# Kernel optimization log

Measured on AMD Instinct MI355X. Metric: run time of the kernel, lower is better.

The kernel has to match this reference:

```python
import jax, jax.numpy as jnp
import numpy as np

# All BatchNorms are in inference mode: folded to per-channel affine (g, b)
# where g = gamma/sqrt(running_var+eps), b = beta - running_mean*g.

def _conv(x, w, stride=1, pad=0, groups=1):
    return jax.lax.conv_general_dilated(
        x, w, (stride, stride), ((pad, pad), (pad, pad)),
        dimension_numbers=('NCHW', 'OIHW', 'NCHW'), feature_group_count=groups)

def _bn(x, g, b):
    return x * g[None, :, None, None] + b[None, :, None, None]

def _gn(x, g, b, eps=1e-5):
    # GroupNorm with 1 group: normalize over (C,H,W) per sample
    m = jnp.mean(x, axis=(1, 2, 3), keepdims=True)
    v = jnp.var(x, axis=(1, 2, 3), keepdims=True)
    return (x - m) * jax.lax.rsqrt(v + eps) * g[None, :, None, None] + b[None, :, None, None]

def _maxpool3(x):
    return jax.lax.reduce_window(x, -jnp.inf, jax.lax.max,
                                 (1, 1, 3, 3), (1, 1, 1, 1),
                                 ((0, 0), (0, 0), (1, 1), (1, 1)))


def reference(x, w_stem, g_stem, b_stem,
              w_cb1, g_cb1, b_cb1, w_cb2, g_cb2, b_cb2, w_cb3, g_cb3, b_cb3,
              w_cbres, g_cbres, b_cbres,
              w_lvc, g_lvc, b_lvc, codewords, cw_scale, g_enc, b_enc,
              w_fc, b_fc,
              gn1_g, gn1_b, w_dw, g_dw, b_dw, w_pw, g_pw, b_pw,
              gn2_g, gn2_b, w_fc1, bias_fc1, w_fc2, bias_fc2, ls1, ls2,
              w_cnv1, b_cnv1):
    relu = jax.nn.relu
    C = x.shape[1]
    # ---- stem: 7x7 conv + BN + ReLU + 3x3 maxpool (stride 1) ----
    x1 = _maxpool3(relu(_bn(_conv(x, w_stem, pad=3), g_stem, b_stem)))

    # ================= LVC branch =================
    # ConvBlock (res_conv=True, stride=1)
    t = relu(_bn(_conv(x1, w_cb1), g_cb1, b_cb1))           # 1x1 C->C/4
    t = relu(_bn(_conv(t, w_cb2, pad=1), g_cb2, b_cb2))     # 3x3 C/4->C/4
    t = _bn(_conv(t, w_cb3), g_cb3, b_cb3)                  # 1x1 C/4->C
    res = _bn(_conv(x1, w_cbres), g_cbres, b_cbres)         # 1x1 residual
    xc = relu(t + res)

    # LVC: 1x1 conv + BN + ReLU -> Encoding -> BN1d -> ReLU -> mean over codes
    z = relu(_bn(_conv(xc, w_lvc), g_lvc, b_lvc))
    b_, _, H, W = z.shape
    zf = z.reshape(b_, C, H * W).transpose(0, 2, 1)         # (b, N, C)
    # scaled L2: scale_k * ||x_n - c_k||^2, expanded (no (b,N,K,C) tensor)
    x2 = jnp.sum(zf * zf, axis=-1, keepdims=True)           # (b, N, 1)
    c2 = jnp.sum(codewords * codewords, axis=-1)            # (K,)
    dist = cw_scale * (x2 - 2.0 * jnp.einsum('bnc,kc->bnk', zf, codewords) + c2)
    A = jax.nn.softmax(dist, axis=2)                        # (b, N, K)
    # aggregate: sum_n A * (x - c) = A^T x - (sum_n A) * c
    en = jnp.einsum('bnk,bnc->bkc', A, zf) - A.sum(axis=1)[..., None] * codewords
    en = relu(en * g_enc[None, :, None] + b_enc[None, :, None])  # BN1d over codes
    en = en.mean(axis=1)                                    # (b, C)
    gam = jax.nn.sigmoid(en @ w_fc.T + b_fc)                # (b, C)
    x_lvc = relu(xc + xc * gam[:, :, None, None])

    # ================= LightMLP branch =================
    h = _gn(x1, gn1_g, gn1_b)
    h = jax.nn.silu(_bn(_conv(h, w_dw, groups=C), g_dw, b_dw))   # depthwise 1x1
    h = jax.nn.silu(_bn(_conv(h, w_pw), g_pw, b_pw))             # pointwise 1x1
    xm = x1 + ls1[None, :, None, None] * h
    h2 = _gn(xm, gn2_g, gn2_b)
    h2 = jax.nn.gelu(_conv(h2, w_fc1) + bias_fc1[None, :, None, None], approximate=False)
    h2 = _conv(h2, w_fc2) + bias_fc2[None, :, None, None]
    xm = xm + ls2[None, :, None, None] * h2

    # ---- fuse: concat + 1x1 conv ----
    out = _conv(jnp.concatenate([x_lvc, xm], axis=1), w_cnv1) + b_cnv1[None, :, None, None]
    return out


def setup_inputs() -> dict:
    B, C, H, W, K = 8, 256, 40, 40, 64
    c = C // 4
    HID = 4 * C
    key = jax.random.key(0)
    ks = iter(jax.random.split(key, 80))
    rn = lambda *s: jax.random.normal(next(ks), s, jnp.float32)
    un = lambda lo, hi, *s: jax.random.uniform(next(ks), s, jnp.float32, lo, hi)

    def aff(n):
        return un(0.8, 1.2, n), rn(n) * 0.1

    d = {}
    d['x'] = rn(B, C, H, W)
    d['w_stem'] = rn(C, C, 7, 7) * 0.01
    d['g_stem'], d['b_stem'] = aff(C)
    d['w_cb1'] = rn(c, C, 1, 1) * 0.05
    d['g_cb1'], d['b_cb1'] = aff(c)
    d['w_cb2'] = rn(c, c, 3, 3) * 0.05
    d['g_cb2'], d['b_cb2'] = aff(c)
    d['w_cb3'] = rn(C, c, 1, 1) * 0.05
    d['g_cb3'], d['b_cb3'] = aff(C)
    d['w_cbres'] = rn(C, C, 1, 1) * 0.05
    d['g_cbres'], d['b_cbres'] = aff(C)
    d['w_lvc'] = rn(C, C, 1, 1) * 0.05
    d['g_lvc'], d['b_lvc'] = aff(C)
    std = 1.0 / (K * C) ** 0.5
    d['codewords'] = un(-std, std, K, C)
    d['cw_scale'] = un(-1.0, 0.0, K)
    d['g_enc'], d['b_enc'] = aff(K)
    d['w_fc'] = rn(C, C) * 0.05
    d['b_fc'] = rn(C) * 0.1
    d['gn1_g'], d['gn1_b'] = aff(C)
    d['w_dw'] = rn(C, 1, 1, 1) * 0.5
    d['g_dw'], d['b_dw'] = aff(C)
    d['w_pw'] = rn(C, C, 1, 1) * 0.05
    d['g_pw'], d['b_pw'] = aff(C)
    d['gn2_g'], d['gn2_b'] = aff(C)
    d['w_fc1'] = rn(HID, C, 1, 1) * 0.05
    d['bias_fc1'] = rn(HID) * 0.02
    d['w_fc2'] = rn(C, HID, 1, 1) * 0.02
    d['bias_fc2'] = rn(C) * 0.02
    d['ls1'] = rn(C) * 0.1
    d['ls2'] = rn(C) * 0.1
    d['w_cnv1'] = rn(C, 2 * C, 1, 1) * 0.04
    d['b_cnv1'] = rn(C) * 0.02
    return d
```

## Files before the change

### kernel.cpp

```cpp
#include <hip/hip_runtime.h>
#include <hip/hip_bf16.h>
#include <math.h>

typedef unsigned short u16;
typedef u16 u16x4 __attribute__((ext_vector_type(4)));
typedef u16 u16x8 __attribute__((ext_vector_type(8)));
typedef short s16x8 __attribute__((ext_vector_type(8)));
typedef float f32x4 __attribute__((ext_vector_type(4)));

#define DEVI static __device__ __forceinline__

DEVI float bf2f(u16 u){ unsigned v=((unsigned)u)<<16; float f; __builtin_memcpy(&f,&v,4); return f; }
DEVI u16 f2bf(float f){ unsigned u; __builtin_memcpy(&u,&f,4); u=(u+0x7FFFu+((u>>16)&1u))>>16; return (u16)u; }

DEVI void gload16(const u16* g, u16* l){
  __builtin_amdgcn_global_load_lds(
      (const __attribute__((address_space(1))) void*)(unsigned long long)g,
      (__attribute__((address_space(3))) void*)(unsigned int)(unsigned long long)l,
      16, 0, 0);
}

constexpr size_t AL(size_t x){ return (x+511)&~(size_t)511; }
constexpr size_t sACT =8ull*1600*256*2;
constexpr size_t oXPAD=0;                constexpr size_t sXPAD=8ull*46*46*256*2;
constexpr size_t oT1P =AL(oXPAD+sXPAD);  constexpr size_t sT1P=8ull*42*42*64*2;
constexpr size_t oSTAT=AL(oT1P+sT1P);    constexpr size_t sSTAT=512;
constexpr size_t ZERO_BYTES=oSTAT+sSTAT;
constexpr size_t oWST =AL(ZERO_BYTES);   constexpr size_t sWST=6553600;
constexpr size_t oWCB2=AL(oWST+sWST);    constexpr size_t sWCB2=9*64*64*2;
constexpr size_t oWSM =AL(oWCB2+sWCB2);  constexpr size_t sWSM=901120ull*2;
constexpr size_t oC2  =AL(oWSM+sWSM);    constexpr size_t sC2=1024;
constexpr size_t oSTEM=AL(oC2+sC2);
constexpr size_t oX1  =AL(oSTEM+sACT);
constexpr size_t oT2  =AL(oX1+sACT);     constexpr size_t sT2=8ull*1600*64*2;
constexpr size_t oRRES=AL(oT2+sT2);
constexpr size_t oXC  =AL(oRRES+sACT);
constexpr size_t oZ   =AL(oXC+sACT);
constexpr size_t oZT  =AL(oZ+sACT);
constexpr size_t oX2  =AL(oZT+sACT);     constexpr size_t sX2=12800*4;
constexpr size_t oDOT =AL(oX2+sX2);      constexpr size_t sDOT=12800ull*64*4;
constexpr size_t oAS  =AL(oDOT+sDOT);    constexpr size_t sAS=64ull*12800*2;
constexpr size_t oASUM=AL(oAS+sAS);      constexpr size_t sASUM=512*4;
constexpr size_t oEN  =AL(oASUM+sASUM);  constexpr size_t sEN=8ull*64*256*4;
constexpr size_t oENM =AL(oEN+sEN);      constexpr size_t sENM=8*256*4;
constexpr size_t oGAM =AL(oENM+sENM);    constexpr size_t sGAM=8*256*4;
constexpr size_t oH2A =AL(oGAM+sGAM);    constexpr size_t sH2A=8ull*1600*1024*2;
constexpr size_t oFUSE=AL(oH2A+sH2A);    constexpr size_t sFUSE=8ull*1600*512*2;
constexpr size_t TOTAL_WS=oFUSE+sFUSE;
static_assert(TOTAL_WS < ((size_t)120<<20), "ws layout ~94MB");
constexpr size_t oPART =oRRES;             constexpr size_t sPART =4ull*12800*256*4;
constexpr size_t oPART2=oPART+sPART;       constexpr size_t sPART2=3ull*12800*64*4;
static_assert(oPART2+sPART2<=TOTAL_WS, "partials fit");

struct WCP { const float* s[9]; u16* d[9]; };
__global__ void wcast_plain(WCP p){
  int idx=blockIdx.x*256+threadIdx.x;
  int j,rel;
  if(idx<16384){j=0;rel=idx;}
  else if(idx<32768){j=1;rel=idx-16384;}
  else if(idx<98304){j=2;rel=idx-32768;}
  else if(idx<163840){j=3;rel=idx-98304;}
  else if(idx<229376){j=4;rel=idx-163840;}
  else if(idx<491520){j=5;rel=idx-229376;}
  else if(idx<753664){j=6;rel=idx-491520;}
  else if(idx<884736){j=7;rel=idx-753664;}
  else if(idx<901120){j=8;rel=idx-884736;}
  else return;
  p.d[j][rel]=f2bf(p.s[j][rel]);
}
__global__ void wcast_stem(const float* __restrict__ w, u16* __restrict__ o){
  __shared__ u16 sh[49*256];
  int co=blockIdx.x, ci=threadIdx.x;
  const float* src=w+(size_t)(co*256+ci)*49;
#pragma unroll 7
  for(int j=0;j<49;j++) sh[j*256+ci]=f2bf(src[j]);
  __syncthreads();
#pragma unroll 7
  for(int j=0;j<49;j++) o[((size_t)j*256+co)*256+ci]=sh[j*256+ci];
}
__global__ void wcast_cb2(const float* __restrict__ w, u16* __restrict__ o){
  int idx=blockIdx.x*256+threadIdx.x;
  if(idx>=9*4096) return;
  int ci=idx&63; int t=idx>>6; int co=t&63; int dhw=t>>6;
  o[idx]=f2bf(w[(co*64+ci)*9+dhw]);
}
__global__ void c2k(const float* __restrict__ cw, float* __restrict__ c2){
  int k=threadIdx.x; if(k>=64) return;
  float s=0.f;
  for(int i=0;i<256;i++){ float v=cw[k*256+i]; s+=v*v; }
  c2[k]=s;
}

__global__ void x_to_xpad(const float* __restrict__ x, u16* __restrict__ xpad){
  __shared__ u16 sh[40*257];
  int h=blockIdx.x, z=blockIdx.y;
  const float* xb=x+(size_t)z*409600+h*40;
  for(int e=threadIdx.x;e<10240;e+=256){ int c=e/40, w=e-40*(e/40); sh[w*257+c]=f2bf(xb[c*1600+w]); }
  __syncthreads();
  u16* op=xpad+((size_t)(z*46+h+3)*46+3)*256;
  for(int e=threadIdx.x;e<10240;e+=256){ int w=e>>8, c=e&255; op[w*256+c]=sh[w*257+c]; }
}

template<int COT,int COTOT,int PXT,int CIN,int PW,int KS,int NW,int TPS,int TTOT>
__global__ __launch_bounds__(NW*64) void conv_lds(
    const u16* __restrict__ Xp, const u16* __restrict__ Wt, float* __restrict__ part){
  constexpr int WPN=PXT/64;
  constexpr int IW=(COT/16)/NW;
  constexpr int IA=(PXT/16)/NW;
  constexpr int CST=CIN/32;
  constexpr int CSH=(CST==8)?3:1;

  __shared__ __align__(16) u16 sW[2][COT*32];
  __shared__ __align__(16) u16 sA[2][PXT*32];

  const int wv=threadIdx.x>>6, ln=threadIdx.x&63, lr=ln&15, kg=ln>>4;
  const int wr=wv/WPN, wc=wv%WPN;
  const int co0=blockIdx.x*COT;
  const int px0=blockIdx.y*PXT;
  const int slice=blockIdx.z;
  const int tb=slice*TPS;
  const int te=(slice==gridDim.z-1)?TTOT:(tb+TPS);
  const int nst=(te-tb)<<CSH;

  int wbase[IW], abase[IA];
#pragma unroll
  for(int q=0;q<IW;q++){
    int wrow=(wv*IW+q)*16+(ln>>2);
    wbase[q]=(co0+wrow)*CIN+(ln&3)*8;
  }
#pragma unroll
  for(int q=0;q<IA;q++){
    int p=px0+(wv*IA+q)*16+(ln>>2);
    int z=p/1600, rem=p-z*1600;
    int h=rem/40, w=rem-h*40;
    abase[q]=((z*PW+h)*PW+w)*CIN+(ln&3)*8;
  }

  f32x4 acc[4][4];
#pragma unroll
  for(int i=0;i<4;i++)
#pragma unroll
    for(int j=0;j<4;j++) acc[i][j]=f32x4{0.f,0.f,0.f,0.f};

  auto stage=[&](int buf,int s){
    int ti=tb+(s>>CSH);
    int c0=(s&(CST-1))<<5;
    int dh=ti/KS, dw=ti-dh*KS;
    const u16* wsrc=Wt+(size_t)ti*COTOT*CIN+c0;
    int aoff=(dh*PW+dw)*CIN+c0;
#pragma unroll
    for(int q=0;q<IW;q++) gload16(wsrc+wbase[q], &sW[buf][(wv*IW+q)*512]);
#pragma unroll
    for(int q=0;q<IA;q++) gload16(Xp+abase[q]+aoff, &sA[buf][(wv*IA+q)*512]);
  };
  auto compute=[&](int buf){
    s16x8 av[4], bv[4];
    const u16* wb=&sW[buf][(wr*64+lr)*32+kg*8];
    const u16* ab=&sA[buf][(wc*64+lr)*32+kg*8];
#pragma unroll
    for(int i=0;i<4;i++) av[i]=*(const s16x8*)(wb+i*512);
#pragma unroll
    for(int j=0;j<4;j++) bv[j]=*(const s16x8*)(ab+j*512);
#pragma unroll
    for(int i=0;i<4;i++)
#pragma unroll
      for(int j=0;j<4;j++)
        acc[i][j]=__builtin_amdgcn_mfma_f32_16x16x32_bf16(av[i],bv[j],acc[i][j],0,0,0);
  };

  stage(0,0);
  for(int s=0;s<nst;s++){
    __syncthreads();
    if(s+1<nst) stage((s+1)&1, s+1);
    compute(s&1);
  }

  float* pb=part+(size_t)slice*12800*COTOT;
#pragma unroll
  for(int i=0;i<4;i++){
    int co=co0+wr*64+i*16+kg*4;
#pragma unroll
    for(int j=0;j<4;j++){
      int px=px0+wc*64+j*16+lr;
      *(f32x4*)(pb+(size_t)px*COTOT+co)=acc[i][j];
    }
  }
}

template<int MT8,int NS>
__global__ void ep_red(const float* __restrict__ part, const float* __restrict__ g,
    const float* __restrict__ b, u16* __restrict__ out){
  int t=blockIdx.x*256+threadIdx.x;
  int c=(t%MT8)*8; int gp=t/MT8;
  size_t base=(size_t)gp*(MT8*8)+c;
  constexpr size_t SS=(size_t)12800*MT8*8;
  f32x4 v0=*(const f32x4*)(part+base), v1=*(const f32x4*)(part+base+4);
#pragma unroll
  for(int s=1;s<NS;s++){
    f32x4 a0=*(const f32x4*)(part+s*SS+base), a1=*(const f32x4*)(part+s*SS+base+4);
#pragma unroll
    for(int q=0;q<4;q++){ v0[q]+=a0[q]; v1[q]+=a1[q]; }
  }
  u16x8 o;
#pragma unroll
  for(int q=0;q<4;q++) o[q]  =f2bf(fmaxf(v0[q]*g[c+q]  +b[c+q],  0.f));
#pragma unroll
  for(int q=0;q<4;q++) o[4+q]=f2bf(fmaxf(v1[q]*g[c+4+q]+b[c+4+q],0.f));
  *(u16x8*)(out+base)=o;
}

__global__ void maxpool3(const u16* __restrict__ in, u16* __restrict__ out){
  int t=blockIdx.x*256+threadIdx.x;
  int c8=(t&31)*8; int gp=t>>5;
  int n=gp%1600; int z=gp/1600; int h=n/40, w=n%40;
  float mx[8];
#pragma unroll
  for(int q=0;q<8;q++) mx[q]=-1e30f;
  for(int dh=-1;dh<=1;dh++){ int hh=h+dh; if((unsigned)hh>=40u) continue;
    for(int dw=-1;dw<=1;dw++){ int ww=w+dw; if((unsigned)ww>=40u) continue;
      u16x8 v=*(const u16x8*)(in+((size_t)z*1600+hh*40+ww)*256+c8);
#pragma unroll
      for(int q=0;q<8;q++) mx[q]=fmaxf(mx[q],bf2f(v[q]));
    }}
  u16x8 o;
#pragma unroll
  for(int q=0;q<8;q++) o[q]=f2bf(mx[q]);
  *(u16x8*)(out+((size_t)z*1600+n)*256+c8)=o;
}

struct GP {
  const u16* A; long long Asz; int lda;
  const u16* Bp; long long Bsz; int ldb;
  int Kd;
  const float *e0,*e1,*e2,*e3;
  const u16* r0;
  u16* ob; float* of; u16* ob2;
  int ldo;
};

template<int MF,int NF,int EPI>
__global__ __launch_bounds__(256) void gemm_nt(GP p){
  const int wv=threadIdx.x>>6, ln=threadIdx.x&63, lr=ln&15, kg=ln>>4;
  int z=blockIdx.z, kc=0;
  if constexpr(EPI==11){ kc=z%5; z=z/5; }
  const int m0=blockIdx.x*(MF*64)+wv*(MF*16);
  const int n0=blockIdx.y*(NF*16);
  const u16* A=p.A+(size_t)z*p.Asz+kc*320;
  const u16* Bb=p.Bp+(size_t)z*p.Bsz+kc*320;
  const u16* ar[MF]; const u16* br[NF];
#pragma unroll
  for(int i=0;i<MF;i++) ar[i]=A+(size_t)(m0+i*16+lr)*p.lda+kg*8;
#pragma unroll
  for(int j=0;j<NF;j++) br[j]=Bb+(size_t)(n0+j*16+lr)*p.ldb+kg*8;
  f32x4 acc[MF][NF];
#pragma unroll
  for(int i=0;i<MF;i++)
#pragma unroll
    for(int j=0;j<NF;j++) acc[i][j]=f32x4{0.f,0.f,0.f,0.f};
  for(int k=0;k<p.Kd;k+=32){
    s16x8 av[MF], bv[NF];
#pragma unroll
    for(int i=0;i<MF;i++) av[i]=*(const s16x8*)(ar[i]+k);
#pragma unroll
    for(int j=0;j<NF;j++) bv[j]=*(const s16x8*)(br[j]+k);
#pragma unroll
    for(int i=0;i<MF;i++)
#pragma unroll
      for(int j=0;j<NF;j++)
        acc[i][j]=__builtin_amdgcn_mfma_f32_16x16x32_bf16(av[i],bv[j],acc[i][j],0,0,0);
  }
#pragma unroll
  for(int i=0;i<MF;i++){
    const int mb=m0+i*16+kg*4;
#pragma unroll
    for(int j=0;j<NF;j++){
      const int n=n0+j*16+lr;
      f32x4 v=acc[i][j];
      if constexpr(EPI==1){
        int h=n/40, w=n%40;
        u16x4 o;
#pragma unroll
        for(int q=0;q<4;q++) o[q]=f2bf(fmaxf(v[q]*p.e0[mb+q]+p.e1[mb+q],0.f));
        *(u16x4*)(p.ob+((size_t)z*1764+(h+1)*42+(w+1))*64+mb)=o;
      } else if constexpr(EPI==2){
        u16x4 o;
#pragma unroll
        for(int q=0;q<4;q++) o[q]=f2bf(v[q]*p.e0[mb+q]+p.e1[mb+q]);
        *(u16x4*)(p.ob+((size_t)z*1600+n)*256+mb)=o;
      } else if constexpr(EPI==3){
        u16x4 rv=*(const u16x4*)(p.r0+((size_t)z*1600+n)*256+mb);
        u16x4 o;
#pragma unroll
        for(int q=0;q<4;q++) o[q]=f2bf(fmaxf(v[q]*p.e0[mb+q]+p.e1[mb+q]+bf2f(rv[q]),0.f));
        *(u16x4*)(p.ob+((size_t)z*1600+n)*256+mb)=o;
      } else if constexpr(EPI==4){
        u16x4 o;
#pragma unroll
        for(int q=0;q<4;q++) o[q]=f2bf(fmaxf(v[q]*p.e0[mb+q]+p.e1[mb+q],0.f));
        *(u16x4*)(p.ob+((size_t)z*1600+n)*256+mb)=o;
#pragma unroll
        for(int q=0;q<4;q++) p.ob2[((size_t)z*256+mb+q)*1600+n]=o[q];
      } else if constexpr(EPI==5){
#pragma unroll
        for(int q=0;q<4;q++) p.of[(size_t)(mb+q)*64+n]=v[q];
      } else if constexpr(EPI==7){
        u16x4 o;
#pragma unroll
        for(int q=0;q<4;q++){ float t=v[q]+p.e0[mb+q]; t=0.5f*t*(1.f+erff(t*0.70710678f)); o[q]=f2bf(t); }
        *(u16x4*)(p.ob+((size_t)z*1600+n)*p.ldo+mb)=o;
      } else if constexpr(EPI==8){
        u16x4 rv=*(const u16x4*)(p.r0+((size_t)z*1600+n)*256+mb);
        u16x4 o;
#pragma unroll
        for(int q=0;q<4;q++){ float t=v[q]+p.e0[mb+q]; o[q]=f2bf(bf2f(rv[q])+p.e1[mb+q]*t); }
        *(u16x4*)(p.ob+((size_t)z*1600+n)*512+mb)=o;
      } else if constexpr(EPI==9){
        u16x4 rv=*(const u16x4*)(p.r0+((size_t)z*1600+n)*256+mb);
        u16x4 o;
#pragma unroll
        for(int q=0;q<4;q++){ float t=v[q]*p.e0[mb+q]+p.e1[mb+q]; float s=t/(1.f+expf(-t));
          o[q]=f2bf(bf2f(rv[q])+p.e2[mb+q]*s); }
        *(u16x4*)(p.ob+((size_t)z*1600+n)*256+mb)=o;
      } else if constexpr(EPI==10){
#pragma unroll
        for(int q=0;q<4;q++) p.of[((size_t)z*256+mb+q)*1600+n]=v[q]+p.e0[mb+q];
      } else if constexpr(EPI==11){
#pragma unroll
        for(int q=0;q<4;q++) atomicAdd(&p.of[((size_t)z*64+mb+q)*256+n],v[q]);
      }
    }
  }
}

__global__ void rowsq(const u16* __restrict__ zb, float* __restrict__ x2){
  int wv=threadIdx.x>>6, ln=threadIdx.x&63;
  int gp=blockIdx.x*4+wv;
  u16x4 v=*(const u16x4*)(zb+(size_t)gp*256+ln*4);
  float s=0.f;
#pragma unroll
  for(int q=0;q<4;q++){ float f=bf2f(v[q]); s+=f*f; }
  for(int d=32;d;d>>=1) s+=__shfl_xor(s,d);
  if(ln==0) x2[gp]=s;
}

__global__ void softmax_k(const float* __restrict__ dot, const float* __restrict__ x2,
    const float* __restrict__ c2, const float* __restrict__ cws, u16* __restrict__ As){
  int wv=threadIdx.x>>6, ln=threadIdx.x&63;
  int base=blockIdx.x*64+wv*16;
  float sc=cws[ln], cc=c2[ln];
  for(int it=0;it<16;it++){
    int gp=base+it;
    float d=sc*(x2[gp]-2.f*dot[(size_t)gp*64+ln]+cc);
    float m=d;
    for(int o=32;o;o>>=1) m=fmaxf(m,__shfl_xor(m,o));
    float e=expf(d-m);
    float s=e;
    for(int o=32;o;o>>=1) s+=__shfl_xor(s,o);
    As[(size_t)ln*12800+gp]=f2bf(e/s);
  }
}

__global__ void asum_k(const u16* __restrict__ As, float* __restrict__ Asum){
  int wv=threadIdx.x>>6, ln=threadIdx.x&63;
  int id=blockIdx.x*4+wv;
  int b=id>>6, k=id&63;
  const u16* r=As+(size_t)k*12800+b*1600;
  float s=0.f;
  for(int i=ln;i<1600;i+=64) s+=bf2f(r[i]);
  for(int o=32;o;o>>=1) s+=__shfl_xor(s,o);
  if(ln==0) Asum[id]=s;
}

__global__ void enmean_ep(const float* __restrict__ enraw, const float* __restrict__ Asum,
    const float* __restrict__ cw, const float* __restrict__ g, const float* __restrict__ b,
    float* __restrict__ enm){
  int bz=blockIdx.x, c=threadIdx.x;
  float s=0.f;
  for(int k=0;k<64;k++){
    float t=(enraw[((size_t)bz*64+k)*256+c]-Asum[bz*64+k]*cw[k*256+c])*g[k]+b[k];
    s+=fmaxf(t,0.f);
  }
  enm[bz*256+c]=s*(1.f/64.f);
}

__global__ void fc_sig(const float* __restrict__ enm, const float* __restrict__ wfc,
    const float* __restrict__ bfc, float* __restrict__ gam){
  __shared__ float sh[256];
  int b=blockIdx.x, co=threadIdx.x;
  sh[co]=enm[b*256+co];
  __syncthreads();
  float s=bfc[co];
  for(int i=0;i<256;i++) s+=sh[i]*wfc[co*256+i];
  gam[b*256+co]=1.f/(1.f+expf(-s));
}

__global__ void ew_xlvc(const u16* __restrict__ xc, const float* __restrict__ gam, u16* __restrict__ fb){
  int t=blockIdx.x*256+threadIdx.x;
  int c=(t&31)*8; int gp=t>>5; int z=gp/1600;
  u16x8 v=*(const u16x8*)(xc+(size_t)gp*256+c);
  u16x8 o;
#pragma unroll
  for(int q=0;q<8;q++){ float ga=1.f+gam[z*256+c+q]; o[q]=f2bf(fmaxf(bf2f(v[q])*ga,0.f)); }
  *(u16x8*)(fb+(size_t)gp*512+c)=o;
}

__global__ void gn_stats(const u16* __restrict__ x, float* __restrict__ st){
  int z=blockIdx.y;
  const u16* pz=x+(size_t)z*409600;
  float s=0.f, ss=0.f;
  for(int i=blockIdx.x*256+threadIdx.x;i<51200;i+=gridDim.x*256){
    u16x8 v=*(const u16x8*)(pz+(size_t)i*8);
#pragma unroll
    for(int q=0;q<8;q++){ float f=bf2f(v[q]); s+=f; ss+=f*f; }
  }
  for(int o=32;o;o>>=1){ s+=__shfl_xor(s,o); ss+=__shfl_xor(ss,o); }
  __shared__ float sh[8];
  int wv=threadIdx.x>>6, ln=threadIdx.x&63;
  if(ln==0){ sh[wv]=s; sh[4+wv]=ss; }
  __syncthreads();
  if(threadIdx.x==0){
    atomicAdd(&st[z*2],  sh[0]+sh[1]+sh[2]+sh[3]);
    atomicAdd(&st[z*2+1],sh[4]+sh[5]+sh[6]+sh[7]);
  }
}

__global__ void ew_hdw(const u16* __restrict__ x1, const float* __restrict__ st,
    const float* __restrict__ g1, const float* __restrict__ b1,
    const float* __restrict__ wdw, const float* __restrict__ gdw, const float* __restrict__ bdw,
    u16* __restrict__ out){
  int t=blockIdx.x*256+threadIdx.x;
  int c=(t&31)*8; int gp=t>>5; int z=gp/1600;
  float mean=st[z*2]*(1.f/409600.f);
  float var=st[z*2+1]*(1.f/409600.f)-mean*mean;
  float rs=rsqrtf(var+1e-5f);
  u16x8 v=*(const u16x8*)(x1+(size_t)gp*256+c);
  u16x8 o;
#pragma unroll
  for(int q=0;q<8;q++){
    int cc=c+q;
    float t0=(bf2f(v[q])-mean)*rs*g1[cc]+b1[cc];
    t0=t0*wdw[cc]*gdw[cc]+bdw[cc];
    o[q]=f2bf(t0/(1.f+expf(-t0)));
  }
  *(u16x8*)(out+(size_t)gp*256+c)=o;
}

__global__ void ew_gn2(const u16* __restrict__ xm, const float* __restrict__ st,
    const float* __restrict__ g2, const float* __restrict__ b2, u16* __restrict__ out){
  int t=blockIdx.x*256+threadIdx.x;
  int c=(t&31)*8; int gp=t>>5; int z=gp/1600;
  float mean=st[z*2]*(1.f/409600.f);
  float var=st[z*2+1]*(1.f/409600.f)-mean*mean;
  float rs=rsqrtf(var+1e-5f);
  u16x8 v=*(const u16x8*)(xm+(size_t)gp*256+c);
  u16x8 o;
#pragma unroll
  for(int q=0;q<8;q++){ int cc=c+q; o[q]=f2bf((bf2f(v[q])-mean)*rs*g2[cc]+b2[cc]); }
  *(u16x8*)(out+(size_t)gp*256+c)=o;
}

extern "C" void kernel_launch(void* const* d_in, const int* in_sizes, int n_in,
                              void* d_out, int out_size, void* d_ws, size_t ws_size,
                              hipStream_t stream){
  const float* X    =(const float*)d_in[0];
  const float* Wstem=(const float*)d_in[1];
  const float* Gstem=(const float*)d_in[2];
  const float* Bstem=(const float*)d_in[3];
  const float* Wcb1 =(const float*)d_in[4];
  const float* Gcb1 =(const float*)d_in[5];
  const float* Bcb1 =(const float*)d_in[6];
  const float* Wcb2 =(const float*)d_in[7];
  const float* Gcb2 =(const float*)d_in[8];
  const float* Bcb2 =(const float*)d_in[9];
  const float* Wcb3 =(const float*)d_in[10];
  const float* Gcb3 =(const float*)d_in[11];
  const float* Bcb3 =(const float*)d_in[12];
  const float* Wres =(const float*)d_in[13];
  const float* Gres =(const float*)d_in[14];
  const float* Bres =(const float*)d_in[15];
  const float* Wlvc =(const float*)d_in[16];
  const float* Glvc =(const float*)d_in[17];
  const float* Blvc =(const float*)d_in[18];
  const float* CW   =(const float*)d_in[19];
  const float* CWS  =(const float*)d_in[20];
  const float* Genc =(const float*)d_in[21];
  const float* Benc =(const float*)d_in[22];
  const float* Wfc  =(const float*)d_in[23];
  const float* Bfc  =(const float*)d_in[24];
  const float* GN1g =(const float*)d_in[25];
  const float* GN1b =(const float*)d_in[26];
  const float* Wdw  =(const float*)d_in[27];
  const float* Gdw  =(const float*)d_in[28];
  const float* Bdw  =(const float*)d_in[29];
  const float* Wpw  =(const float*)d_in[30];
  const float* Gpw  =(const float*)d_in[31];
  const float* Bpw  =(const float*)d_in[32];
  const float* GN2g =(const float*)d_in[33];
  const float* GN2b =(const float*)d_in[34];
  const float* Wfc1 =(const float*)d_in[35];
  const float* Bfc1 =(const float*)d_in[36];
  const float* Wfc2 =(const float*)d_in[37];
  const float* Bfc2 =(const float*)d_in[38];
  const float* LS1  =(const float*)d_in[39];
  const float* LS2  =(const float*)d_in[40];
  const float* Wcnv =(const float*)d_in[41];
  const float* Bcnv =(const float*)d_in[42];
  char* ws=(char*)d_ws;
  if(ws_size < TOTAL_WS) return;

  u16* xpad=(u16*)(ws+oXPAD);
  u16* t1p =(u16*)(ws+oT1P);
  float* stats=(float*)(ws+oSTAT);
  u16* wst =(u16*)(ws+oWST);
  u16* wcb2t=(u16*)(ws+oWCB2);
  u16* wsm =(u16*)(ws+oWSM);
  float* c2b=(float*)(ws+oC2);
  u16* act =(u16*)(ws+oSTEM);
  u16* x1  =(u16*)(ws+oX1);
  u16* t2  =(u16*)(ws+oT2);
  u16* rres=(u16*)(ws+oRRES);
  u16* xc  =(u16*)(ws+oXC);
  u16* zb  =(u16*)(ws+oZ);
  u16* zt  =(u16*)(ws+oZT);
  float* x2b=(float*)(ws+oX2);
  float* dotb=(float*)(ws+oDOT);
  u16* As  =(u16*)(ws+oAS);
  float* Asum=(float*)(ws+oASUM);
  float* enraw=(float*)(ws+oEN);
  float* enm=(float*)(ws+oENM);
  float* gam=(float*)(ws+oGAM);
  u16* h2a =(u16*)(ws+oH2A);
  u16* fb  =(u16*)(ws+oFUSE);
  u16* xm  =(u16*)(ws+oXPAD);
  u16* xmgn=(u16*)(ws+oWST);
  u16* hdw =(u16*)(ws+oRRES);
  float* accP =(float*)(ws+oPART);
  float* accP2=(float*)(ws+oPART2);
  u16* wcb1=wsm+0;      u16* wcb3=wsm+16384;  u16* wresb=wsm+32768; u16* wlvcb=wsm+98304;
  u16* wpwb=wsm+163840; u16* wfc1b=wsm+229376;u16* wfc2b=wsm+491520;u16* wcnvb=wsm+753664;
  u16* cwb=wsm+884736;

  hipMemsetAsync(d_ws,0,ZERO_BYTES,stream);
  { WCP p;
    p.s[0]=Wcb1;p.d[0]=wcb1;  p.s[1]=Wcb3;p.d[1]=wcb3;  p.s[2]=Wres;p.d[2]=wresb;
    p.s[3]=Wlvc;p.d[3]=wlvcb; p.s[4]=Wpw;p.d[4]=wpwb;   p.s[5]=Wfc1;p.d[5]=wfc1b;
    p.s[6]=Wfc2;p.d[6]=wfc2b; p.s[7]=Wcnv;p.d[7]=wcnvb; p.s[8]=CW;p.d[8]=cwb;
    wcast_plain<<<3520,256,0,stream>>>(p); }
  wcast_stem<<<256,256,0,stream>>>(Wstem,wst);
  wcast_cb2<<<144,256,0,stream>>>(Wcb2,wcb2t);
  c2k<<<1,64,0,stream>>>(CW,c2b);
  x_to_xpad<<<dim3(40,8),256,0,stream>>>(X,xpad);

  conv_lds<128,256,128,256,46,7,4,12,49><<<dim3(2,100,4),256,0,stream>>>(xpad,wst,accP);
  ep_red<32,4><<<1600,256,0,stream>>>(accP,Gstem,Bstem,act);
  maxpool3<<<1600,256,0,stream>>>(act,x1);

  { GP p{}; p.A=wcb1;p.Asz=0;p.lda=256; p.Bp=x1;p.Bsz=1600*256;p.ldb=256; p.Kd=256;
    p.e0=Gcb1;p.e1=Bcb1; p.ob=t1p;
    gemm_nt<1,5,1><<<dim3(1,20,8),256,0,stream>>>(p); }
  conv_lds<64,64,128,64,42,3,2,3,9><<<dim3(1,100,3),128,0,stream>>>(t1p,wcb2t,accP2);
  ep_red<8,3><<<400,256,0,stream>>>(accP2,Gcb2,Bcb2,t2);
  { GP p{}; p.A=wresb;p.Asz=0;p.lda=256; p.Bp=x1;p.Bsz=1600*256;p.ldb=256; p.Kd=256;
    p.e0=Gres;p.e1=Bres; p.ob=rres;
    gemm_nt<2,5,2><<<dim3(2,20,8),256,0,stream>>>(p); }
  { GP p{}; p.A=wcb3;p.Asz=0;p.lda=64; p.Bp=t2;p.Bsz=1600*64;p.ldb=64; p.Kd=64;
    p.e0=Gcb3;p.e1=Bcb3; p.r0=rres; p.ob=xc;
    gemm_nt<2,5,3><<<dim3(2,20,8),256,0,stream>>>(p); }
  { GP p{}; p.A=wlvcb;p.Asz=0;p.lda=256; p.Bp=xc;p.Bsz=1600*256;p.ldb=256; p.Kd=256;
    p.e0=Glvc;p.e1=Blvc; p.ob=zb; p.ob2=zt;
    gemm_nt<2,5,4><<<dim3(2,20,8),256,0,stream>>>(p); }
  rowsq<<<3200,256,0,stream>>>(zb,x2b);
  { GP p{}; p.A=zb;p.Asz=0;p.lda=256; p.Bp=cwb;p.Bsz=0;p.ldb=256; p.Kd=256; p.of=dotb;
    gemm_nt<2,4,5><<<dim3(100,1,1),256,0,stream>>>(p); }
  softmax_k<<<200,256,0,stream>>>(dotb,x2b,c2b,CWS,As);
  asum_k<<<128,256,0,stream>>>(As,Asum);
  hipMemsetAsync(enraw,0,sEN,stream);
  { GP p{}; p.A=As;p.Asz=1600;p.lda=12800; p.Bp=zt;p.Bsz=256*1600;p.ldb=1600; p.Kd=320;
    p.of=enraw;
    gemm_nt<1,4,11><<<dim3(1,4,40),256,0,stream>>>(p); }
  enmean_ep<<<8,256,0,stream>>>(enraw,Asum,CW,Genc,Benc,enm);
  fc_sig<<<8,256,0,stream>>>(enm,Wfc,Bfc,gam);
  ew_xlvc<<<1600,256,0,stream>>>(xc,gam,fb);

  gn_stats<<<dim3(25,8),256,0,stream>>>(x1,stats);
  ew_hdw<<<1600,256,0,stream>>>(x1,stats,GN1g,GN1b,Wdw,Gdw,Bdw,hdw);
  { GP p{}; p.A=wpwb;p.Asz=0;p.lda=256; p.Bp=hdw;p.Bsz=1600*256;p.ldb=256; p.Kd=256;
    p.e0=Gpw;p.e1=Bpw;p.e2=LS1; p.r0=x1; p.ob=xm;
    gemm_nt<2,5,9><<<dim3(2,20,8),256,0,stream>>>(p); }
  gn_stats<<<dim3(25,8),256,0,stream>>>(xm,stats+16);
  ew_gn2<<<1600,256,0,stream>>>(xm,stats+16,GN2g,GN2b,xmgn);
  { GP p{}; p.A=wfc1b;p.Asz=0;p.lda=256; p.Bp=xmgn;p.Bsz=1600*256;p.ldb=256; p.Kd=256;
    p.e0=Bfc1; p.ob=h2a; p.ldo=1024;
    gemm_nt<2,5,7><<<dim3(8,20,8),256,0,stream>>>(p); }
  { GP p{}; p.A=wfc2b;p.Asz=0;p.lda=1024; p.Bp=h2a;p.Bsz=1600*1024;p.ldb=1024; p.Kd=1024;
    p.e0=Bfc2;p.e1=LS2; p.r0=xm; p.ob=fb+256;
    gemm_nt<2,5,8><<<dim3(2,20,8),256,0,stream>>>(p); }
  { GP p{}; p.A=wcnvb;p.Asz=0;p.lda=512; p.Bp=fb;p.Bsz=1600*512;p.ldb=512; p.Kd=512;
    p.e0=Bcnv; p.of=(float*)d_out;
    gemm_nt<2,5,10><<<dim3(2,20,8),256,0,stream>>>(p); }
}
```

Before: 653.2 us.

## Retile GEMMs to smaller tiles, swizzle stem conv blocks across XCDs, relayout LDS

```diff
diff --git a/kernel.cpp b/kernel.cpp
--- a/kernel.cpp
+++ b/kernel.cpp
@@ -101,12 +101,14 @@
   for(int e=threadIdx.x;e<10240;e+=256){ int w=e>>8, c=e&255; op[w*256+c]=sh[w*257+c]; }
 }
 
-template<int COT,int COTOT,int PXT,int CIN,int PW,int KS,int NW,int TPS,int TTOT>
+template<int COT,int COTOT,int PXT,int CIN,int PW,int KS,int NW,int TPS,int TTOT,int NSLICE,int XSWZ>
 __global__ __launch_bounds__(NW*64) void conv_lds(
     const u16* __restrict__ Xp, const u16* __restrict__ Wt, float* __restrict__ part){
   constexpr int WPN=PXT/64;
-  constexpr int IW=(COT/16)/NW;
-  constexpr int IA=(PXT/16)/NW;
+  constexpr int WGR=COT/16;
+  constexpr int AGR=PXT/16;
+  constexpr int IW=WGR/NW;
+  constexpr int IA=AGR/NW;
   constexpr int CST=CIN/32;
   constexpr int CSH=(CST==8)?3:1;
 
@@ -115,25 +117,30 @@
 
   const int wv=threadIdx.x>>6, ln=threadIdx.x&63, lr=ln&15, kg=ln>>4;
   const int wr=wv/WPN, wc=wv%WPN;
-  const int co0=blockIdx.x*COT;
-  const int px0=blockIdx.y*PXT;
-  const int slice=blockIdx.z;
+  int co0,px0,slice;
+  if constexpr(XSWZ){
+    int lin=blockIdx.x; int xcd=lin&7, grp=lin>>3;
+    slice=xcd>>1; co0=(xcd&1)*COT; px0=grp*PXT;
+  } else {
+    co0=blockIdx.x*COT; px0=blockIdx.y*PXT; slice=blockIdx.z;
+  }
   const int tb=slice*TPS;
-  const int te=(slice==gridDim.z-1)?TTOT:(tb+TPS);
+  const int te=(slice==NSLICE-1)?TTOT:(tb+TPS);
   const int nst=(te-tb)<<CSH;
 
   int wbase[IW], abase[IA];
 #pragma unroll
   for(int q=0;q<IW;q++){
-    int wrow=(wv*IW+q)*16+(ln>>2);
-    wbase[q]=(co0+wrow)*CIN+(ln&3)*8;
+    int g=wv*IW+q;
+    wbase[q]=(co0+g*16+lr)*CIN+kg*8;
   }
 #pragma unroll
   for(int q=0;q<IA;q++){
-    int p=px0+(wv*IA+q)*16+(ln>>2);
+    int g=wv*IA+q;
+    int p=px0+g*16+lr;
     int z=p/1600, rem=p-z*1600;
     int h=rem/40, w=rem-h*40;
-    abase[q]=((z*PW+h)*PW+w)*CIN+(ln&3)*8;
+    abase[q]=((z*PW+h)*PW+w)*CIN+kg*8;
   }
 
   f32x4 acc[4][4];
@@ -155,12 +162,10 @@
   };
   auto compute=[&](int buf){
     s16x8 av[4], bv[4];
-    const u16* wb=&sW[buf][(wr*64+lr)*32+kg*8];
-    const u16* ab=&sA[buf][(wc*64+lr)*32+kg*8];
-#pragma unroll
-    for(int i=0;i<4;i++) av[i]=*(const s16x8*)(wb+i*512);
-#pragma unroll
-    for(int j=0;j<4;j++) bv[j]=*(const s16x8*)(ab+j*512);
+#pragma unroll
+    for(int i=0;i<4;i++) av[i]=*(const s16x8*)(&sW[buf][(wr*4+i)*512+ln*8]);
+#pragma unroll
+    for(int j=0;j<4;j++) bv[j]=*(const s16x8*)(&sA[buf][(wc*4+j)*512+ln*8]);
 #pragma unroll
     for(int i=0;i<4;i++)
 #pragma unroll
@@ -257,6 +262,7 @@
   for(int i=0;i<MF;i++)
 #pragma unroll
     for(int j=0;j<NF;j++) acc[i][j]=f32x4{0.f,0.f,0.f,0.f};
+#pragma unroll 2
   for(int k=0;k<p.Kd;k+=32){
     s16x8 av[MF], bv[NF];
 #pragma unroll
@@ -551,27 +557,27 @@
   c2k<<<1,64,0,stream>>>(CW,c2b);
   x_to_xpad<<<dim3(40,8),256,0,stream>>>(X,xpad);
 
-  conv_lds<128,256,128,256,46,7,4,12,49><<<dim3(2,100,4),256,0,stream>>>(xpad,wst,accP);
+  conv_lds<128,256,128,256,46,7,4,12,49,4,1><<<800,256,0,stream>>>(xpad,wst,accP);
   ep_red<32,4><<<1600,256,0,stream>>>(accP,Gstem,Bstem,act);
   maxpool3<<<1600,256,0,stream>>>(act,x1);
 
   { GP p{}; p.A=wcb1;p.Asz=0;p.lda=256; p.Bp=x1;p.Bsz=1600*256;p.ldb=256; p.Kd=256;
     p.e0=Gcb1;p.e1=Bcb1; p.ob=t1p;
-    gemm_nt<1,5,1><<<dim3(1,20,8),256,0,stream>>>(p); }
-  conv_lds<64,64,128,64,42,3,2,3,9><<<dim3(1,100,3),128,0,stream>>>(t1p,wcb2t,accP2);
+    gemm_nt<1,4,1><<<dim3(1,25,8),256,0,stream>>>(p); }
+  conv_lds<64,64,128,64,42,3,2,3,9,3,0><<<dim3(1,100,3),128,0,stream>>>(t1p,wcb2t,accP2);
   ep_red<8,3><<<400,256,0,stream>>>(accP2,Gcb2,Bcb2,t2);
   { GP p{}; p.A=wresb;p.Asz=0;p.lda=256; p.Bp=x1;p.Bsz=1600*256;p.ldb=256; p.Kd=256;
     p.e0=Gres;p.e1=Bres; p.ob=rres;
-    gemm_nt<2,5,2><<<dim3(2,20,8),256,0,stream>>>(p); }
+    gemm_nt<1,4,2><<<dim3(4,25,8),256,0,stream>>>(p); }
   { GP p{}; p.A=wcb3;p.Asz=0;p.lda=64; p.Bp=t2;p.Bsz=1600*64;p.ldb=64; p.Kd=64;
     p.e0=Gcb3;p.e1=Bcb3; p.r0=rres; p.ob=xc;
-    gemm_nt<2,5,3><<<dim3(2,20,8),256,0,stream>>>(p); }
+    gemm_nt<1,4,3><<<dim3(4,25,8),256,0,stream>>>(p); }
   { GP p{}; p.A=wlvcb;p.Asz=0;p.lda=256; p.Bp=xc;p.Bsz=1600*256;p.ldb=256; p.Kd=256;
     p.e0=Glvc;p.e1=Blvc; p.ob=zb; p.ob2=zt;
-    gemm_nt<2,5,4><<<dim3(2,20,8),256,0,stream>>>(p); }
+    gemm_nt<1,4,4><<<dim3(4,25,8),256,0,stream>>>(p); }
   rowsq<<<3200,256,0,stream>>>(zb,x2b);
   { GP p{}; p.A=zb;p.Asz=0;p.lda=256; p.Bp=cwb;p.Bsz=0;p.ldb=256; p.Kd=256; p.of=dotb;
-    gemm_nt<2,4,5><<<dim3(100,1,1),256,0,stream>>>(p); }
+    gemm_nt<1,4,5><<<dim3(200,1,1),256,0,stream>>>(p); }
   softmax_k<<<200,256,0,stream>>>(dotb,x2b,c2b,CWS,As);
   asum_k<<<128,256,0,stream>>>(As,Asum);
   hipMemsetAsync(enraw,0,sEN,stream);
@@ -586,16 +592,16 @@
   ew_hdw<<<1600,256,0,stream>>>(x1,stats,GN1g,GN1b,Wdw,Gdw,Bdw,hdw);
   { GP p{}; p.A=wpwb;p.Asz=0;p.lda=256; p.Bp=hdw;p.Bsz=1600*256;p.ldb=256; p.Kd=256;
     p.e0=Gpw;p.e1=Bpw;p.e2=LS1; p.r0=x1; p.ob=xm;
-    gemm_nt<2,5,9><<<dim3(2,20,8),256,0,stream>>>(p); }
+    gemm_nt<1,4,9><<<dim3(4,25,8),256,0,stream>>>(p); }
   gn_stats<<<dim3(25,8),256,0,stream>>>(xm,stats+16);
   ew_gn2<<<1600,256,0,stream>>>(xm,stats+16,GN2g,GN2b,xmgn);
   { GP p{}; p.A=wfc1b;p.Asz=0;p.lda=256; p.Bp=xmgn;p.Bsz=1600*256;p.ldb=256; p.Kd=256;
     p.e0=Bfc1; p.ob=h2a; p.ldo=1024;
-    gemm_nt<2,5,7><<<dim3(8,20,8),256,0,stream>>>(p); }
+    gemm_nt<1,4,7><<<dim3(16,25,8),256,0,stream>>>(p); }
   { GP p{}; p.A=wfc2b;p.Asz=0;p.lda=1024; p.Bp=h2a;p.Bsz=1600*1024;p.ldb=1024; p.Kd=1024;
     p.e0=Bfc2;p.e1=LS2; p.r0=xm; p.ob=fb+256;
-    gemm_nt<2,5,8><<<dim3(2,20,8),256,0,stream>>>(p); }
+    gemm_nt<1,4,8><<<dim3(4,25,8),256,0,stream>>>(p); }
   { GP p{}; p.A=wcnvb;p.Asz=0;p.lda=512; p.Bp=fb;p.Bsz=1600*512;p.ldb=512; p.Kd=512;
     p.e0=Bcnv; p.of=(float*)d_out;
-    gemm_nt<2,5,10><<<dim3(2,20,8),256,0,stream>>>(p); }
-}
+    gemm_nt<1,4,10><<<dim3(4,25,8),256,0,stream>>>(p); }
+}
```

Result: slower. 775.8 us (+18.8%).
